# Kernel optimization log

Hardware: AMD Instinct MI355X
Metric: run time of the kernel (lower is better)

The kernel has to match this reference:

```python
import jax, jax.numpy as jnp
import numpy as np

B, S, D = 2, 2048, 768
H = 12
HD = D // H  # head_dim = 64
WINDOW = 128
NEG = -1e9


def setup_inputs() -> dict:
    key = jax.random.key(0)
    k1, k2, k3 = jax.random.split(key, 3)
    x = jax.random.normal(k1, (B, S, D), dtype=jnp.float32)
    padding_mask = jnp.ones((B, S), dtype=jnp.float32)
    Wqkv = jax.random.normal(k2, (D, 3 * D), dtype=jnp.float32) * (1.0 / np.sqrt(D))
    Wo = jax.random.normal(k3, (D, D), dtype=jnp.float32) * (1.0 / np.sqrt(D))
    return {"x": x, "padding_mask": padding_mask, "Wqkv": Wqkv, "Wo": Wo}


def reference(x, padding_mask, Wqkv, Wo):
    b, s = x.shape[0], x.shape[1]
    qkv = x @ Wqkv  # [b, s, 3D]
    qkv = qkv.reshape(b, s, 3, H, HD)
    q = qkv[:, :, 0]  # [b, s, H, HD]
    k = qkv[:, :, 1]
    v = qkv[:, :, 2]
    # scores: [b, H, s, s]
    scores = jnp.einsum("bqhd,bkhd->bhqk", q, k) / jnp.sqrt(jnp.asarray(HD, x.dtype))
    # sliding-window additive mask
    idx = jnp.arange(s)
    sw_mask = (jnp.abs(idx[:, None] - idx[None, :]) <= WINDOW // 2).astype(jnp.float32)
    scores = scores + (1.0 - sw_mask)[None, None, :, :] * NEG
    # padding mask over keys
    scores = scores + (1.0 - padding_mask)[:, None, None, :] * NEG
    attn = jax.nn.softmax(scores, axis=-1)
    out = jnp.einsum("bhqk,bkhd->bqhd", attn, v).reshape(b, s, D)
    return out @ Wo
```

## Files before the change

### kernel.cpp

```cpp
#include <hip/hip_runtime.h>
#include <stdint.h>

typedef short bf16x8 __attribute__((ext_vector_type(8)));
typedef float f32x4 __attribute__((ext_vector_type(4)));

#define SEQ_ 2048
#define DM_ 768
#define NH_ 12

__device__ __forceinline__ unsigned short f2bf(float f) {
  unsigned int u = __float_as_uint(f);
  u += 0x7fffu + ((u >> 16) & 1u);
  return (unsigned short)(u >> 16);
}

__device__ __forceinline__ void load_lds16(const unsigned short* g, unsigned short* l) {
  __builtin_amdgcn_global_load_lds((__attribute__((address_space(1))) void*)g,
                                   (__attribute__((address_space(3))) void*)l, 16, 0, 0);
}

__device__ __forceinline__ void transpose_body(const float* __restrict__ src,
                                               unsigned short* __restrict__ dst,
                                               int R, int C, int bx, int by,
                                               float (*t)[65]) {
  int c0 = bx << 6, r0 = by << 6;
  int tid = threadIdx.x;
#pragma unroll
  for (int i = 0; i < 4; i++) {
    int e = (i * 256 + tid) * 4;
    int r = e >> 6, c = e & 63;
    float4 v = *(const float4*)(src + (size_t)(r0 + r) * C + c0 + c);
    t[r][c] = v.x; t[r][c + 1] = v.y; t[r][c + 2] = v.z; t[r][c + 3] = v.w;
  }
  __syncthreads();
#pragma unroll
  for (int i = 0; i < 4; i++) {
    int e = (i * 256 + tid) * 4;
    int r = e >> 6, c = e & 63;
    unsigned short o4[4];
#pragma unroll
    for (int j = 0; j < 4; j++) o4[j] = f2bf(t[c + j][r]);
    *(uint2*)(dst + (size_t)(c0 + r) * R + r0 + c) = *(const uint2*)o4;
  }
}

__global__ __launch_bounds__(256) void prep(const float* __restrict__ x,
                                            const float* __restrict__ Wqkv,
                                            const float* __restrict__ Wo,
                                            unsigned short* __restrict__ xb,
                                            unsigned short* __restrict__ wqkvt,
                                            unsigned short* __restrict__ wot) {
  __shared__ float t[64][65];
  int blk = blockIdx.x;
  if (blk < 3072) {
    int i = (blk * 256 + threadIdx.x) * 4;
    float4 v = *(const float4*)(x + i);
    unsigned short o[4] = {f2bf(v.x), f2bf(v.y), f2bf(v.z), f2bf(v.w)};
    *(uint2*)(xb + i) = *(const uint2*)o;
  } else if (blk < 3072 + 432) {
    int idx = blk - 3072;
    transpose_body(Wqkv, wqkvt, DM_, 3 * DM_, idx % 36, idx / 36, t);
  } else {
    int idx = blk - 3504;
    transpose_body(Wo, wot, DM_, DM_, idx % 12, idx / 12, t);
  }
}

__global__ __launch_bounds__(256, 3) void gemm_qkv(const unsigned short* __restrict__ A,
                                                   const unsigned short* __restrict__ Bt,
                                                   unsigned short* __restrict__ Qb,
                                                   unsigned short* __restrict__ Kb,
                                                   unsigned short* __restrict__ Vtb) {
  const int K = 768;
  __shared__ unsigned short smem[128 * 64 + 96 * 64];
  unsigned short* As = smem;
  unsigned short* Bs = smem + 128 * 64;
  f32x4 acc[4][3];
  f32x4 z = {0.f, 0.f, 0.f, 0.f};
#pragma unroll
  for (int i = 0; i < 4; i++)
#pragma unroll
    for (int j = 0; j < 3; j++) acc[i][j] = z;
  int m0 = blockIdx.x << 7, n0 = blockIdx.y * 96;
  int tid = threadIdx.x, wv = tid >> 6, ln = tid & 63, quad = ln >> 4, lrow = ln & 15;
  int row = tid >> 3;
  int col8 = (tid & 7) ^ (row & 7);
  const unsigned short* a0 = A + (size_t)(m0 + row) * K + col8 * 8;
  const unsigned short* b0 = Bt + (size_t)(n0 + row) * K + col8 * 8;
  int mw = (wv >> 1) << 6, nw = (wv & 1) * 48;
  int sw = lrow & 7;
  for (int kt = 0; kt < K; kt += 64) {
#pragma unroll
    for (int st = 0; st < 4; st++)
      load_lds16(a0 + (size_t)(st * 32) * K + kt, As + (st * 256 + tid) * 8);
#pragma unroll
    for (int st = 0; st < 3; st++)
      load_lds16(b0 + (size_t)(st * 32) * K + kt, Bs + (st * 256 + tid) * 8);
    __syncthreads();
#pragma unroll
    for (int ks = 0; ks < 2; ks++) {
      bf16x8 af[4], bfr[3];
#pragma unroll
      for (int i = 0; i < 4; i++)
        af[i] = *(const bf16x8*)(As + (mw + i * 16 + lrow) * 64 + (((ks * 4 + quad) ^ sw) << 3));
#pragma unroll
      for (int j = 0; j < 3; j++)
        bfr[j] = *(const bf16x8*)(Bs + (nw + j * 16 + lrow) * 64 + (((ks * 4 + quad) ^ sw) << 3));
#pragma unroll
      for (int i = 0; i < 4; i++)
#pragma unroll
        for (int j = 0; j < 3; j++)
          acc[i][j] = __builtin_amdgcn_mfma_f32_16x16x32_bf16(af[i], bfr[j], acc[i][j], 0, 0, 0);
    }
    __syncthreads();
  }
  int mw_l = mw, nw_l = nw;
  int bb = m0 >> 11;
  int which = n0 / DM_;
  int nrem0 = n0 - which * DM_;
  if (which < 2) {
    unsigned short* dstp = which == 0 ? Qb : Kb;
#pragma unroll
    for (int j = 0; j < 3; j++) {
      int nb = nrem0 + nw_l + j * 16;
      int h = nb >> 6, hdb = (nb & 63) + lrow;
      size_t hoff = (size_t)(bb * NH_ + h) << 11;
#pragma unroll
      for (int i = 0; i < 4; i++)
#pragma unroll
        for (int r = 0; r < 4; r++) {
          int s = (m0 + mw_l + i * 16 + quad * 4 + r) & (SEQ_ - 1);
          dstp[((hoff + s) << 6) + hdb] = f2bf(acc[i][j][r]);
        }
    }
  } else {
    const int LSTR = 136;
    int hdl2 = ((wv & 1) << 4) + lrow;
    int hds = tid >> 3, s0 = (tid & 7) << 4;
    int hd_in_block = (hds & 16) * 3 + (hds & 15);
#pragma unroll
    for (int j = 0; j < 3; j++) {
      __syncthreads();
#pragma unroll
      for (int i = 0; i < 4; i++)
#pragma unroll
        for (int r = 0; r < 4; r++) {
          int sl = mw_l + i * 16 + quad * 4 + r;
          smem[hdl2 * LSTR + sl] = f2bf(acc[i][j][r]);
        }
      __syncthreads();
      int nb = nrem0 + hd_in_block + j * 16;
      int h = nb >> 6, hdh = nb & 63;
      uint4 p0 = *(const uint4*)&smem[hds * LSTR + s0];
      uint4 p1 = *(const uint4*)&smem[hds * LSTR + s0 + 8];
      size_t vbase = (size_t)(((bb * NH_ + h) << 6) + hdh) * SEQ_ + (m0 & (SEQ_ - 1)) + s0;
      *(uint4*)(Vtb + vbase) = p0;
      *(uint4*)(Vtb + vbase + 8) = p1;
    }
  }
}

__global__ __launch_bounds__(256, 3) void gemm_out(const unsigned short* __restrict__ A,
                                                   const unsigned short* __restrict__ Bt,
                                                   float* __restrict__ out) {
  const int K = 768;
  __shared__ __align__(16) unsigned char sraw[64 * 100 * 4];
  unsigned short* As = (unsigned short*)sraw;
  unsigned short* Bs = As + 64 * 64;
  f32x4 acc[2][3];
  f32x4 z = {0.f, 0.f, 0.f, 0.f};
#pragma unroll
  for (int i = 0; i < 2; i++)
#pragma unroll
    for (int j = 0; j < 3; j++) acc[i][j] = z;
  int m0 = blockIdx.x << 6, n0 = blockIdx.y * 96;
  int tid = threadIdx.x, wv = tid >> 6, ln = tid & 63, quad = ln >> 4, lrow = ln & 15;
  int row = tid >> 3;
  int col8 = (tid & 7) ^ (row & 7);
  const unsigned short* a0 = A + (size_t)(m0 + row) * K + col8 * 8;
  const unsigned short* b0 = Bt + (size_t)(n0 + row) * K + col8 * 8;
  int mw = (wv >> 1) << 5, nw = (wv & 1) * 48;
  int sw = lrow & 7;
  for (int kt = 0; kt < K; kt += 64) {
#pragma unroll
    for (int st = 0; st < 2; st++)
      load_lds16(a0 + (size_t)(st * 32) * K + kt, As + (st * 256 + tid) * 8);
#pragma unroll
    for (int st = 0; st < 3; st++)
      load_lds16(b0 + (size_t)(st * 32) * K + kt, Bs + (st * 256 + tid) * 8);
    __syncthreads();
#pragma unroll
    for (int ks = 0; ks < 2; ks++) {
      bf16x8 af[2], bfr[3];
#pragma unroll
      for (int i = 0; i < 2; i++)
        af[i] = *(const bf16x8*)(As + (mw + i * 16 + lrow) * 64 + (((ks * 4 + quad) ^ sw) << 3));
#pragma unroll
      for (int j = 0; j < 3; j++)
        bfr[j] = *(const bf16x8*)(Bs + (nw + j * 16 + lrow) * 64 + (((ks * 4 + quad) ^ sw) << 3));
#pragma unroll
      for (int i = 0; i < 2; i++)
#pragma unroll
        for (int j = 0; j < 3; j++)
          acc[i][j] = __builtin_amdgcn_mfma_f32_16x16x32_bf16(af[i], bfr[j], acc[i][j], 0, 0, 0);
    }
    __syncthreads();
  }
  float* fs = (float*)sraw;
  __syncthreads();
#pragma unroll
  for (int i = 0; i < 2; i++)
#pragma unroll
    for (int j = 0; j < 3; j++)
#pragma unroll
      for (int r = 0; r < 4; r++)
        fs[(mw + i * 16 + quad * 4 + r) * 100 + nw + j * 16 + lrow] = acc[i][j][r];
  __syncthreads();
#pragma unroll
  for (int rd = 0; rd < 6; rd++) {
    int idx = rd * 256 + tid;
    int r_ = idx / 24, c4 = idx % 24;
    float4 v = *(const float4*)&fs[r_ * 100 + c4 * 4];
    *(float4*)(out + (size_t)(m0 + r_) * DM_ + n0 + c4 * 4) = v;
  }
}

__global__ __launch_bounds__(256, 3) void attn_kernel(const unsigned short* __restrict__ Qb,
                                                      const unsigned short* __restrict__ Kb,
                                                      const unsigned short* __restrict__ Vtb,
                                                      const float* __restrict__ pmask,
                                                      unsigned short* __restrict__ Obf) {
  __shared__ unsigned short Ps[4][16 * 168];
  int blk = blockIdx.x;
  int tile = blk & 31, bh = blk >> 5;
  int b = bh / NH_, h = bh % NH_;
  int q0 = tile << 6;
  int kstart = q0 - 64;
  int tid = threadIdx.x, wv = tid >> 6, ln = tid & 63, quad = ln >> 4, lrow = ln & 15;
  int kb = wv << 4;
  int qw = q0 + (wv << 4);

  const unsigned short* Qg = Qb + ((size_t)bh << 11) * 64;
  const unsigned short* Kg = Kb + ((size_t)bh << 11) * 64;
  const unsigned short* Vg = Vtb + ((size_t)bh << 6) * SEQ_;

  bf16x8 qf0 = *(const bf16x8*)(Qg + (qw + lrow) * 64 + quad * 8);
  bf16x8 qf1 = *(const bf16x8*)(Qg + (qw + lrow) * 64 + 32 + quad * 8);

  float sc[9][4];
#pragma unroll
  for (int t = 0; t < 9; t++) {
    int kg = kstart + kb + t * 16 + lrow;
    int kgc = kg < 0 ? 0 : (kg > SEQ_ - 1 ? SEQ_ - 1 : kg);
    bf16x8 kf0 = *(const bf16x8*)(Kg + (size_t)kgc * 64 + quad * 8);
    bf16x8 kf1 = *(const bf16x8*)(Kg + (size_t)kgc * 64 + 32 + quad * 8);
    f32x4 c = {0.f, 0.f, 0.f, 0.f};
    c = __builtin_amdgcn_mfma_f32_16x16x32_bf16(qf0, kf0, c, 0, 0, 0);
    c = __builtin_amdgcn_mfma_f32_16x16x32_bf16(qf1, kf1, c, 0, 0, 0);
    float pv = pmask[(b << 11) + kgc];
    bool valid = (kg >= 0) & (kg < SEQ_);
    float mneg = (valid && pv != 0.0f) ? 0.0f : -1e30f;
#pragma unroll
    for (int r = 0; r < 4; r++) {
      int qr = quad * 4 + r;
      float w = mneg;
      if (t == 0) w = (lrow >= qr) ? w : -1e30f;
      if (t == 8) w = (lrow <= qr) ? w : -1e30f;
      sc[t][r] = c[r] * 0.125f + w;
    }
  }
  float inv[4];
#pragma unroll
  for (int r = 0; r < 4; r++) {
    float mx = sc[0][r];
#pragma unroll
    for (int t = 1; t < 9; t++) mx = fmaxf(mx, sc[t][r]);
    mx = fmaxf(mx, __shfl_xor(mx, 1));
    mx = fmaxf(mx, __shfl_xor(mx, 2));
    mx = fmaxf(mx, __shfl_xor(mx, 4));
    mx = fmaxf(mx, __shfl_xor(mx, 8));
    float s = 0.f;
#pragma unroll
    for (int t = 0; t < 9; t++) {
      sc[t][r] = __expf(sc[t][r] - mx);
      s += sc[t][r];
    }
    s += __shfl_xor(s, 1);
    s += __shfl_xor(s, 2);
    s += __shfl_xor(s, 4);
    s += __shfl_xor(s, 8);
    inv[r] = 1.0f / s;
  }
  unsigned short* Pw = &Ps[wv][0];
#pragma unroll
  for (int t = 0; t < 9; t++)
#pragma unroll
    for (int r = 0; r < 4; r++)
      Pw[(quad * 4 + r) * 168 + t * 16 + lrow] = f2bf(sc[t][r] * inv[r]);
  {
    int prow = ln >> 2, c0 = 144 + (ln & 3) * 4;
    uint2 zz; zz.x = 0; zz.y = 0;
    *(uint2*)(Pw + prow * 168 + c0) = zz;
  }
  __syncthreads();
  f32x4 o[4];
  f32x4 z = {0.f, 0.f, 0.f, 0.f};
#pragma unroll
  for (int tt = 0; tt < 4; tt++) o[tt] = z;
#pragma unroll
  for (int ks = 0; ks < 5; ks++) {
    bf16x8 pf = *(const bf16x8*)(Pw + lrow * 168 + ks * 32 + quad * 8);
    int kg = kstart + kb + ks * 32 + quad * 8;
    int kgc = kg < 0 ? 0 : (kg > SEQ_ - 8 ? SEQ_ - 8 : kg);
#pragma unroll
    for (int tt = 0; tt < 4; tt++) {
      bf16x8 vf = *(const bf16x8*)(Vg + (size_t)(tt * 16 + lrow) * SEQ_ + kgc);
      o[tt] = __builtin_amdgcn_mfma_f32_16x16x32_bf16(pf, vf, o[tt], 0, 0, 0);
    }
  }
#pragma unroll
  for (int tt = 0; tt < 4; tt++)
#pragma unroll
    for (int r = 0; r < 4; r++) {
      int s_ = qw + quad * 4 + r;
      Obf[((size_t)(b << 11) + s_) * DM_ + h * 64 + tt * 16 + lrow] = f2bf(o[tt][r]);
    }
}

extern "C" void kernel_launch(void* const* d_in, const int* in_sizes, int n_in,
                              void* d_out, int out_size, void* d_ws, size_t ws_size,
                              hipStream_t stream) {
  const float* x = (const float*)d_in[0];
  const float* pmask = (const float*)d_in[1];
  const float* Wqkv = (const float*)d_in[2];
  const float* Wo = (const float*)d_in[3];
  float* out = (float*)d_out;
  char* ws = (char*)d_ws;

  unsigned short* xb    = (unsigned short*)(ws + 0);
  unsigned short* wqkvt = (unsigned short*)(ws + 6291456);
  unsigned short* wot   = (unsigned short*)(ws + 9830400);
  unsigned short* Qb    = (unsigned short*)(ws + 11010048);
  unsigned short* Kb    = (unsigned short*)(ws + 17301504);
  unsigned short* Vtb   = (unsigned short*)(ws + 23592960);
  unsigned short* attn_bf = xb;

  prep<<<3648, 256, 0, stream>>>(x, Wqkv, Wo, xb, wqkvt, wot);
  gemm_qkv<<<dim3(32, 24), 256, 0, stream>>>(xb, wqkvt, Qb, Kb, Vtb);
  attn_kernel<<<768, 256, 0, stream>>>(Qb, Kb, Vtb, pmask, attn_bf);
  gemm_out<<<dim3(64, 8), 256, 0, stream>>>(attn_bf, wot, out);
}
```

Measured before the change: 120.7 us.

## Fuse QKV GEMM, attention and output GEMM into one persistent kernel with grid barriers

Merges the QKV projection, sliding-window attention and output projection into a single 768-block kernel. The stages are separated by an atomic-counter grid barrier, with a counter memset added before launch. This removes two kernel launches and the gaps between them. The attention softmax also drops the max subtraction and defers normalization to the output write, and the output GEMM now uses 64x64 tiles so its grid matches the 768 blocks. The barrier relies on all blocks being resident at once. Skipping the max subtraction can overflow exp if scores get large.

```diff
diff --git a/kernel.cpp b/kernel.cpp
--- a/kernel.cpp
+++ b/kernel.cpp
@@ -17,6 +17,18 @@
 __device__ __forceinline__ void load_lds16(const unsigned short* g, unsigned short* l) {
   __builtin_amdgcn_global_load_lds((__attribute__((address_space(1))) void*)g,
                                    (__attribute__((address_space(3))) void*)l, 16, 0, 0);
+}
+
+__device__ __forceinline__ void gridbar(unsigned* cnt, unsigned target) {
+  __syncthreads();
+  if (threadIdx.x == 0) {
+    __threadfence();
+    atomicAdd(cnt, 1u);
+    while (__hip_atomic_load(cnt, __ATOMIC_RELAXED, __HIP_MEMORY_SCOPE_AGENT) < target)
+      __builtin_amdgcn_s_sleep(2);
+    __threadfence();
+  }
+  __syncthreads();
 }
 
 __device__ __forceinline__ void transpose_body(const float* __restrict__ src,
@@ -66,265 +78,254 @@
   }
 }
 
-__global__ __launch_bounds__(256, 3) void gemm_qkv(const unsigned short* __restrict__ A,
-                                                   const unsigned short* __restrict__ Bt,
-                                                   unsigned short* __restrict__ Qb,
-                                                   unsigned short* __restrict__ Kb,
-                                                   unsigned short* __restrict__ Vtb) {
-  const int K = 768;
-  __shared__ unsigned short smem[128 * 64 + 96 * 64];
-  unsigned short* As = smem;
-  unsigned short* Bs = smem + 128 * 64;
-  f32x4 acc[4][3];
-  f32x4 z = {0.f, 0.f, 0.f, 0.f};
-#pragma unroll
-  for (int i = 0; i < 4; i++)
-#pragma unroll
-    for (int j = 0; j < 3; j++) acc[i][j] = z;
-  int m0 = blockIdx.x << 7, n0 = blockIdx.y * 96;
-  int tid = threadIdx.x, wv = tid >> 6, ln = tid & 63, quad = ln >> 4, lrow = ln & 15;
-  int row = tid >> 3;
-  int col8 = (tid & 7) ^ (row & 7);
-  const unsigned short* a0 = A + (size_t)(m0 + row) * K + col8 * 8;
-  const unsigned short* b0 = Bt + (size_t)(n0 + row) * K + col8 * 8;
-  int mw = (wv >> 1) << 6, nw = (wv & 1) * 48;
-  int sw = lrow & 7;
-  for (int kt = 0; kt < K; kt += 64) {
-#pragma unroll
-    for (int st = 0; st < 4; st++)
-      load_lds16(a0 + (size_t)(st * 32) * K + kt, As + (st * 256 + tid) * 8);
-#pragma unroll
-    for (int st = 0; st < 3; st++)
-      load_lds16(b0 + (size_t)(st * 32) * K + kt, Bs + (st * 256 + tid) * 8);
+__global__ __launch_bounds__(256, 3) void fused(const float* __restrict__ pmask,
+                                                float* __restrict__ out,
+                                                unsigned short* __restrict__ xb,
+                                                const unsigned short* __restrict__ wqkvt,
+                                                const unsigned short* __restrict__ wot,
+                                                unsigned short* __restrict__ Qb,
+                                                unsigned short* __restrict__ Kb,
+                                                unsigned short* __restrict__ Vtb,
+                                                unsigned* __restrict__ cnt) {
+  __shared__ __align__(16) unsigned char sraw[28672];
+  unsigned short* smem = (unsigned short*)sraw;
+  int bid = blockIdx.x, tid = threadIdx.x;
+  int wv = tid >> 6, ln = tid & 63, quad = ln >> 4, lrow = ln & 15;
+
+  {
+    const int K = 768;
+    unsigned short* As = smem;
+    unsigned short* Bs = smem + 128 * 64;
+    f32x4 acc[4][3];
+    f32x4 z = {0.f, 0.f, 0.f, 0.f};
+#pragma unroll
+    for (int i = 0; i < 4; i++)
+#pragma unroll
+      for (int j = 0; j < 3; j++) acc[i][j] = z;
+    int m0 = (bid & 31) << 7, n0 = (bid >> 5) * 96;
+    int row = tid >> 3;
+    int col8 = (tid & 7) ^ (row & 7);
+    const unsigned short* a0 = xb + (size_t)(m0 + row) * K + col8 * 8;
+    const unsigned short* b0 = wqkvt + (size_t)(n0 + row) * K + col8 * 8;
+    int mw = (wv >> 1) << 6, nw = (wv & 1) * 48;
+    int sw = lrow & 7;
+    for (int kt = 0; kt < K; kt += 64) {
+#pragma unroll
+      for (int st = 0; st < 4; st++)
+        load_lds16(a0 + (size_t)(st * 32) * K + kt, As + (st * 256 + tid) * 8);
+#pragma unroll
+      for (int st = 0; st < 3; st++)
+        load_lds16(b0 + (size_t)(st * 32) * K + kt, Bs + (st * 256 + tid) * 8);
+      __syncthreads();
+#pragma unroll
+      for (int ks = 0; ks < 2; ks++) {
+        bf16x8 af[4], bfr[3];
+#pragma unroll
+        for (int i = 0; i < 4; i++)
+          af[i] = *(const bf16x8*)(As + (mw + i * 16 + lrow) * 64 + (((ks * 4 + quad) ^ sw) << 3));
+#pragma unroll
+        for (int j = 0; j < 3; j++)
+          bfr[j] = *(const bf16x8*)(Bs + (nw + j * 16 + lrow) * 64 + (((ks * 4 + quad) ^ sw) << 3));
+#pragma unroll
+        for (int i = 0; i < 4; i++)
+#pragma unroll
+          for (int j = 0; j < 3; j++)
+            acc[i][j] = __builtin_amdgcn_mfma_f32_16x16x32_bf16(af[i], bfr[j], acc[i][j], 0, 0, 0);
+      }
+      __syncthreads();
+    }
+    int bb = m0 >> 11;
+    int which = n0 / DM_;
+    int nrem0 = n0 - which * DM_;
+    if (which < 2) {
+      unsigned short* dstp = which == 0 ? Qb : Kb;
+#pragma unroll
+      for (int j = 0; j < 3; j++) {
+        int nb = nrem0 + nw + j * 16;
+        int h = nb >> 6, hdb = (nb & 63) + lrow;
+        size_t hoff = (size_t)(bb * NH_ + h) << 11;
+#pragma unroll
+        for (int i = 0; i < 4; i++)
+#pragma unroll
+          for (int r = 0; r < 4; r++) {
+            int s = (m0 + mw + i * 16 + quad * 4 + r) & (SEQ_ - 1);
+            dstp[((hoff + s) << 6) + hdb] = f2bf(acc[i][j][r]);
+          }
+      }
+    } else {
+      const int LSTR = 136;
+      int hdl2 = ((wv & 1) << 4) + lrow;
+      int hds = tid >> 3, s0 = (tid & 7) << 4;
+      int hd_in_block = (hds & 16) * 3 + (hds & 15);
+#pragma unroll
+      for (int j = 0; j < 3; j++) {
+        __syncthreads();
+#pragma unroll
+        for (int i = 0; i < 4; i++)
+#pragma unroll
+          for (int r = 0; r < 4; r++) {
+            int sl = mw + i * 16 + quad * 4 + r;
+            smem[hdl2 * LSTR + sl] = f2bf(acc[i][j][r]);
+          }
+        __syncthreads();
+        int nb = nrem0 + hd_in_block + j * 16;
+        int h = nb >> 6, hdh = nb & 63;
+        uint4 p0 = *(const uint4*)&smem[hds * LSTR + s0];
+        uint4 p1 = *(const uint4*)&smem[hds * LSTR + s0 + 8];
+        size_t vbase = (size_t)(((bb * NH_ + h) << 6) + hdh) * SEQ_ + (m0 & (SEQ_ - 1)) + s0;
+        *(uint4*)(Vtb + vbase) = p0;
+        *(uint4*)(Vtb + vbase + 8) = p1;
+      }
+    }
+  }
+  gridbar(cnt, 768);
+
+  {
+    unsigned short* Pw = smem + wv * (16 * 168);
+    int tile = bid & 31, bh = bid >> 5;
+    int b = bh / NH_, h = bh % NH_;
+    int q0 = tile << 6;
+    int kstart = q0 - 64;
+    int kb = wv << 4;
+    int qw = q0 + (wv << 4);
+
+    const unsigned short* Qg = Qb + ((size_t)bh << 11) * 64;
+    const unsigned short* Kg = Kb + ((size_t)bh << 11) * 64;
+    const unsigned short* Vg = Vtb + ((size_t)bh << 6) * SEQ_;
+
+    bf16x8 qf0 = *(const bf16x8*)(Qg + (qw + lrow) * 64 + quad * 8);
+    bf16x8 qf1 = *(const bf16x8*)(Qg + (qw + lrow) * 64 + 32 + quad * 8);
+
+    float sc[9][4];
+#pragma unroll
+    for (int t = 0; t < 9; t++) {
+      int kg = kstart + kb + t * 16 + lrow;
+      int kgc = kg < 0 ? 0 : (kg > SEQ_ - 1 ? SEQ_ - 1 : kg);
+      bf16x8 kf0 = *(const bf16x8*)(Kg + (size_t)kgc * 64 + quad * 8);
+      bf16x8 kf1 = *(const bf16x8*)(Kg + (size_t)kgc * 64 + 32 + quad * 8);
+      f32x4 c = {0.f, 0.f, 0.f, 0.f};
+      c = __builtin_amdgcn_mfma_f32_16x16x32_bf16(qf0, kf0, c, 0, 0, 0);
+      c = __builtin_amdgcn_mfma_f32_16x16x32_bf16(qf1, kf1, c, 0, 0, 0);
+      float pv = pmask[(b << 11) + kgc];
+      bool valid = (kg >= 0) & (kg < SEQ_);
+      float mneg = (valid && pv != 0.0f) ? 0.0f : -1e30f;
+#pragma unroll
+      for (int r = 0; r < 4; r++) {
+        int qr = quad * 4 + r;
+        float w = mneg;
+        if (t == 0) w = (lrow >= qr) ? w : -1e30f;
+        if (t == 8) w = (lrow <= qr) ? w : -1e30f;
+        sc[t][r] = __expf(c[r] * 0.125f + w);
+      }
+    }
+    float inv[4];
+#pragma unroll
+    for (int r = 0; r < 4; r++) {
+      float s = 0.f;
+#pragma unroll
+      for (int t = 0; t < 9; t++) s += sc[t][r];
+      s += __shfl_xor(s, 1);
+      s += __shfl_xor(s, 2);
+      s += __shfl_xor(s, 4);
+      s += __shfl_xor(s, 8);
+      inv[r] = 1.0f / s;
+    }
+#pragma unroll
+    for (int t = 0; t < 9; t++)
+#pragma unroll
+      for (int r = 0; r < 4; r++)
+        Pw[(quad * 4 + r) * 168 + t * 16 + lrow] = f2bf(sc[t][r]);
+    {
+      int prow = ln >> 2, c0 = 144 + (ln & 3) * 4;
+      uint2 zz; zz.x = 0; zz.y = 0;
+      *(uint2*)(Pw + prow * 168 + c0) = zz;
+    }
     __syncthreads();
-#pragma unroll
-    for (int ks = 0; ks < 2; ks++) {
-      bf16x8 af[4], bfr[3];
-#pragma unroll
-      for (int i = 0; i < 4; i++)
-        af[i] = *(const bf16x8*)(As + (mw + i * 16 + lrow) * 64 + (((ks * 4 + quad) ^ sw) << 3));
-#pragma unroll
-      for (int j = 0; j < 3; j++)
-        bfr[j] = *(const bf16x8*)(Bs + (nw + j * 16 + lrow) * 64 + (((ks * 4 + quad) ^ sw) << 3));
-#pragma unroll
-      for (int i = 0; i < 4; i++)
-#pragma unroll
-        for (int j = 0; j < 3; j++)
-          acc[i][j] = __builtin_amdgcn_mfma_f32_16x16x32_bf16(af[i], bfr[j], acc[i][j], 0, 0, 0);
-    }
+    f32x4 o[4];
+    f32x4 z = {0.f, 0.f, 0.f, 0.f};
+#pragma unroll
+    for (int tt = 0; tt < 4; tt++) o[tt] = z;
+#pragma unroll
+    for (int ks = 0; ks < 5; ks++) {
+      bf16x8 pf = *(const bf16x8*)(Pw + lrow * 168 + ks * 32 + quad * 8);
+      int kg = kstart + kb + ks * 32 + quad * 8;
+      int kgc = kg < 0 ? 0 : (kg > SEQ_ - 8 ? SEQ_ - 8 : kg);
+#pragma unroll
+      for (int tt = 0; tt < 4; tt++) {
+        bf16x8 vf = *(const bf16x8*)(Vg + (size_t)(tt * 16 + lrow) * SEQ_ + kgc);
+        o[tt] = __builtin_amdgcn_mfma_f32_16x16x32_bf16(pf, vf, o[tt], 0, 0, 0);
+      }
+    }
+#pragma unroll
+    for (int tt = 0; tt < 4; tt++)
+#pragma unroll
+      for (int r = 0; r < 4; r++) {
+        int s_ = qw + quad * 4 + r;
+        xb[((size_t)(b << 11) + s_) * DM_ + h * 64 + tt * 16 + lrow] = f2bf(o[tt][r] * inv[r]);
+      }
     __syncthreads();
   }
-  int mw_l = mw, nw_l = nw;
-  int bb = m0 >> 11;
-  int which = n0 / DM_;
-  int nrem0 = n0 - which * DM_;
-  if (which < 2) {
-    unsigned short* dstp = which == 0 ? Qb : Kb;
-#pragma unroll
-    for (int j = 0; j < 3; j++) {
-      int nb = nrem0 + nw_l + j * 16;
-      int h = nb >> 6, hdb = (nb & 63) + lrow;
-      size_t hoff = (size_t)(bb * NH_ + h) << 11;
-#pragma unroll
-      for (int i = 0; i < 4; i++)
-#pragma unroll
-        for (int r = 0; r < 4; r++) {
-          int s = (m0 + mw_l + i * 16 + quad * 4 + r) & (SEQ_ - 1);
-          dstp[((hoff + s) << 6) + hdb] = f2bf(acc[i][j][r]);
-        }
-    }
-  } else {
-    const int LSTR = 136;
-    int hdl2 = ((wv & 1) << 4) + lrow;
-    int hds = tid >> 3, s0 = (tid & 7) << 4;
-    int hd_in_block = (hds & 16) * 3 + (hds & 15);
-#pragma unroll
-    for (int j = 0; j < 3; j++) {
+  gridbar(cnt, 1536);
+
+  {
+    const int K = 768;
+    unsigned short* As = smem;
+    unsigned short* Bs = smem + 4096;
+    f32x4 acc[2][2];
+    f32x4 z = {0.f, 0.f, 0.f, 0.f};
+#pragma unroll
+    for (int i = 0; i < 2; i++)
+#pragma unroll
+      for (int j = 0; j < 2; j++) acc[i][j] = z;
+    int m0 = (bid & 63) << 6, n0 = (bid >> 6) << 6;
+    int row = tid >> 3;
+    int col8 = (tid & 7) ^ (row & 7);
+    const unsigned short* a0 = xb + (size_t)(m0 + row) * K + col8 * 8;
+    const unsigned short* b0 = wot + (size_t)(n0 + row) * K + col8 * 8;
+    int mw = (wv >> 1) << 5, nw = (wv & 1) << 5;
+    int sw = lrow & 7;
+    for (int kt = 0; kt < K; kt += 64) {
+#pragma unroll
+      for (int st = 0; st < 2; st++) {
+        load_lds16(a0 + (size_t)(st * 32) * K + kt, As + (st * 256 + tid) * 8);
+        load_lds16(b0 + (size_t)(st * 32) * K + kt, Bs + (st * 256 + tid) * 8);
+      }
       __syncthreads();
 #pragma unroll
-      for (int i = 0; i < 4; i++)
-#pragma unroll
-        for (int r = 0; r < 4; r++) {
-          int sl = mw_l + i * 16 + quad * 4 + r;
-          smem[hdl2 * LSTR + sl] = f2bf(acc[i][j][r]);
-        }
+      for (int ks = 0; ks < 2; ks++) {
+        bf16x8 af[2], bfr[2];
+#pragma unroll
+        for (int i = 0; i < 2; i++)
+          af[i] = *(const bf16x8*)(As + (mw + i * 16 + lrow) * 64 + (((ks * 4 + quad) ^ sw) << 3));
+#pragma unroll
+        for (int j = 0; j < 2; j++)
+          bfr[j] = *(const bf16x8*)(Bs + (nw + j * 16 + lrow) * 64 + (((ks * 4 + quad) ^ sw) << 3));
+#pragma unroll
+        for (int i = 0; i < 2; i++)
+#pragma unroll
+          for (int j = 0; j < 2; j++)
+            acc[i][j] = __builtin_amdgcn_mfma_f32_16x16x32_bf16(af[i], bfr[j], acc[i][j], 0, 0, 0);
+      }
       __syncthreads();
-      int nb = nrem0 + hd_in_block + j * 16;
-      int h = nb >> 6, hdh = nb & 63;
-      uint4 p0 = *(const uint4*)&smem[hds * LSTR + s0];
-      uint4 p1 = *(const uint4*)&smem[hds * LSTR + s0 + 8];
-      size_t vbase = (size_t)(((bb * NH_ + h) << 6) + hdh) * SEQ_ + (m0 & (SEQ_ - 1)) + s0;
-      *(uint4*)(Vtb + vbase) = p0;
-      *(uint4*)(Vtb + vbase + 8) = p1;
-    }
-  }
-}
-
-__global__ __launch_bounds__(256, 3) void gemm_out(const unsigned short* __restrict__ A,
-                                                   const unsigned short* __restrict__ Bt,
-                                                   float* __restrict__ out) {
-  const int K = 768;
-  __shared__ __align__(16) unsigned char sraw[64 * 100 * 4];
-  unsigned short* As = (unsigned short*)sraw;
-  unsigned short* Bs = As + 64 * 64;
-  f32x4 acc[2][3];
-  f32x4 z = {0.f, 0.f, 0.f, 0.f};
-#pragma unroll
-  for (int i = 0; i < 2; i++)
-#pragma unroll
-    for (int j = 0; j < 3; j++) acc[i][j] = z;
-  int m0 = blockIdx.x << 6, n0 = blockIdx.y * 96;
-  int tid = threadIdx.x, wv = tid >> 6, ln = tid & 63, quad = ln >> 4, lrow = ln & 15;
-  int row = tid >> 3;
-  int col8 = (tid & 7) ^ (row & 7);
-  const unsigned short* a0 = A + (size_t)(m0 + row) * K + col8 * 8;
-  const unsigned short* b0 = Bt + (size_t)(n0 + row) * K + col8 * 8;
-  int mw = (wv >> 1) << 5, nw = (wv & 1) * 48;
-  int sw = lrow & 7;
-  for (int kt = 0; kt < K; kt += 64) {
-#pragma unroll
-    for (int st = 0; st < 2; st++)
-      load_lds16(a0 + (size_t)(st * 32) * K + kt, As + (st * 256 + tid) * 8);
-#pragma unroll
-    for (int st = 0; st < 3; st++)
-      load_lds16(b0 + (size_t)(st * 32) * K + kt, Bs + (st * 256 + tid) * 8);
+    }
+    float* fs = (float*)sraw;
     __syncthreads();
 #pragma unroll
-    for (int ks = 0; ks < 2; ks++) {
-      bf16x8 af[2], bfr[3];
-#pragma unroll
-      for (int i = 0; i < 2; i++)
-        af[i] = *(const bf16x8*)(As + (mw + i * 16 + lrow) * 64 + (((ks * 4 + quad) ^ sw) << 3));
-#pragma unroll
-      for (int j = 0; j < 3; j++)
-        bfr[j] = *(const bf16x8*)(Bs + (nw + j * 16 + lrow) * 64 + (((ks * 4 + quad) ^ sw) << 3));
-#pragma unroll
-      for (int i = 0; i < 2; i++)
-#pragma unroll
-        for (int j = 0; j < 3; j++)
-          acc[i][j] = __builtin_amdgcn_mfma_f32_16x16x32_bf16(af[i], bfr[j], acc[i][j], 0, 0, 0);
-    }
+    for (int i = 0; i < 2; i++)
+#pragma unroll
+      for (int j = 0; j < 2; j++)
+#pragma unroll
+        for (int r = 0; r < 4; r++)
+          fs[(mw + i * 16 + quad * 4 + r) * 68 + nw + j * 16 + lrow] = acc[i][j][r];
     __syncthreads();
-  }
-  float* fs = (float*)sraw;
-  __syncthreads();
-#pragma unroll
-  for (int i = 0; i < 2; i++)
-#pragma unroll
-    for (int j = 0; j < 3; j++)
-#pragma unroll
-      for (int r = 0; r < 4; r++)
-        fs[(mw + i * 16 + quad * 4 + r) * 100 + nw + j * 16 + lrow] = acc[i][j][r];
-  __syncthreads();
-#pragma unroll
-  for (int rd = 0; rd < 6; rd++) {
-    int idx = rd * 256 + tid;
-    int r_ = idx / 24, c4 = idx % 24;
-    float4 v = *(const float4*)&fs[r_ * 100 + c4 * 4];
-    *(float4*)(out + (size_t)(m0 + r_) * DM_ + n0 + c4 * 4) = v;
-  }
-}
-
-__global__ __launch_bounds__(256, 3) void attn_kernel(const unsigned short* __restrict__ Qb,
-                                                      const unsigned short* __restrict__ Kb,
-                                                      const unsigned short* __restrict__ Vtb,
-                                                      const float* __restrict__ pmask,
-                                                      unsigned short* __restrict__ Obf) {
-  __shared__ unsigned short Ps[4][16 * 168];
-  int blk = blockIdx.x;
-  int tile = blk & 31, bh = blk >> 5;
-  int b = bh / NH_, h = bh % NH_;
-  int q0 = tile << 6;
-  int kstart = q0 - 64;
-  int tid = threadIdx.x, wv = tid >> 6, ln = tid & 63, quad = ln >> 4, lrow = ln & 15;
-  int kb = wv << 4;
-  int qw = q0 + (wv << 4);
-
-  const unsigned short* Qg = Qb + ((size_t)bh << 11) * 64;
-  const unsigned short* Kg = Kb + ((size_t)bh << 11) * 64;
-  const unsigned short* Vg = Vtb + ((size_t)bh << 6) * SEQ_;
-
-  bf16x8 qf0 = *(const bf16x8*)(Qg + (qw + lrow) * 64 + quad * 8);
-  bf16x8 qf1 = *(const bf16x8*)(Qg + (qw + lrow) * 64 + 32 + quad * 8);
-
-  float sc[9][4];
-#pragma unroll
-  for (int t = 0; t < 9; t++) {
-    int kg = kstart + kb + t * 16 + lrow;
-    int kgc = kg < 0 ? 0 : (kg > SEQ_ - 1 ? SEQ_ - 1 : kg);
-    bf16x8 kf0 = *(const bf16x8*)(Kg + (size_t)kgc * 64 + quad * 8);
-    bf16x8 kf1 = *(const bf16x8*)(Kg + (size_t)kgc * 64 + 32 + quad * 8);
-    f32x4 c = {0.f, 0.f, 0.f, 0.f};
-    c = __builtin_amdgcn_mfma_f32_16x16x32_bf16(qf0, kf0, c, 0, 0, 0);
-    c = __builtin_amdgcn_mfma_f32_16x16x32_bf16(qf1, kf1, c, 0, 0, 0);
-    float pv = pmask[(b << 11) + kgc];
-    bool valid = (kg >= 0) & (kg < SEQ_);
-    float mneg = (valid && pv != 0.0f) ? 0.0f : -1e30f;
-#pragma unroll
-    for (int r = 0; r < 4; r++) {
-      int qr = quad * 4 + r;
-      float w = mneg;
-      if (t == 0) w = (lrow >= qr) ? w : -1e30f;
-      if (t == 8) w = (lrow <= qr) ? w : -1e30f;
-      sc[t][r] = c[r] * 0.125f + w;
-    }
-  }
-  float inv[4];
-#pragma unroll
-  for (int r = 0; r < 4; r++) {
-    float mx = sc[0][r];
-#pragma unroll
-    for (int t = 1; t < 9; t++) mx = fmaxf(mx, sc[t][r]);
-    mx = fmaxf(mx, __shfl_xor(mx, 1));
-    mx = fmaxf(mx, __shfl_xor(mx, 2));
-    mx = fmaxf(mx, __shfl_xor(mx, 4));
-    mx = fmaxf(mx, __shfl_xor(mx, 8));
-    float s = 0.f;
-#pragma unroll
-    for (int t = 0; t < 9; t++) {
-      sc[t][r] = __expf(sc[t][r] - mx);
-      s += sc[t][r];
-    }
-    s += __shfl_xor(s, 1);
-    s += __shfl_xor(s, 2);
-    s += __shfl_xor(s, 4);
-    s += __shfl_xor(s, 8);
-    inv[r] = 1.0f / s;
-  }
-  unsigned short* Pw = &Ps[wv][0];
-#pragma unroll
-  for (int t = 0; t < 9; t++)
-#pragma unroll
-    for (int r = 0; r < 4; r++)
-      Pw[(quad * 4 + r) * 168 + t * 16 + lrow] = f2bf(sc[t][r] * inv[r]);
-  {
-    int prow = ln >> 2, c0 = 144 + (ln & 3) * 4;
-    uint2 zz; zz.x = 0; zz.y = 0;
-    *(uint2*)(Pw + prow * 168 + c0) = zz;
-  }
-  __syncthreads();
-  f32x4 o[4];
-  f32x4 z = {0.f, 0.f, 0.f, 0.f};
-#pragma unroll
-  for (int tt = 0; tt < 4; tt++) o[tt] = z;
-#pragma unroll
-  for (int ks = 0; ks < 5; ks++) {
-    bf16x8 pf = *(const bf16x8*)(Pw + lrow * 168 + ks * 32 + quad * 8);
-    int kg = kstart + kb + ks * 32 + quad * 8;
-    int kgc = kg < 0 ? 0 : (kg > SEQ_ - 8 ? SEQ_ - 8 : kg);
-#pragma unroll
-    for (int tt = 0; tt < 4; tt++) {
-      bf16x8 vf = *(const bf16x8*)(Vg + (size_t)(tt * 16 + lrow) * SEQ_ + kgc);
-      o[tt] = __builtin_amdgcn_mfma_f32_16x16x32_bf16(pf, vf, o[tt], 0, 0, 0);
-    }
-  }
-#pragma unroll
-  for (int tt = 0; tt < 4; tt++)
-#pragma unroll
-    for (int r = 0; r < 4; r++) {
-      int s_ = qw + quad * 4 + r;
-      Obf[((size_t)(b << 11) + s_) * DM_ + h * 64 + tt * 16 + lrow] = f2bf(o[tt][r]);
-    }
+#pragma unroll
+    for (int rd = 0; rd < 4; rd++) {
+      int idx = rd * 256 + tid;
+      int r_ = idx >> 4, c4 = idx & 15;
+      float4 v = *(const float4*)&fs[r_ * 68 + c4 * 4];
+      *(float4*)(out + (size_t)(m0 + r_) * DM_ + n0 + c4 * 4) = v;
+    }
+  }
 }
 
 extern "C" void kernel_launch(void* const* d_in, const int* in_sizes, int n_in,
@@ -343,10 +344,9 @@
   unsigned short* Qb    = (unsigned short*)(ws + 11010048);
   unsigned short* Kb    = (unsigned short*)(ws + 17301504);
   unsigned short* Vtb   = (unsigned short*)(ws + 23592960);
-  unsigned short* attn_bf = xb;
-
+  unsigned* cnt         = (unsigned*)(ws + 29884416);
+
+  hipMemsetAsync(cnt, 0, 64, stream);
   prep<<<3648, 256, 0, stream>>>(x, Wqkv, Wo, xb, wqkvt, wot);
-  gemm_qkv<<<dim3(32, 24), 256, 0, stream>>>(xb, wqkvt, Qb, Kb, Vtb);
-  attn_kernel<<<768, 256, 0, stream>>>(Qb, Kb, Vtb, pmask, attn_bf);
-  gemm_out<<<dim3(64, 8), 256, 0, stream>>>(attn_bf, wot, out);
-}
+  fused<<<768, 256, 0, stream>>>(pmask, out, xb, wqkvt, wot, Qb, Kb, Vtb, cnt);
+}
```

After: 302.2 us. 2.5x slower.
